# Optimization experiments

Hardware: AMD Instinct MI355X
Metric: run time of the kernel (lower is better)

Reference implementation:

```python
import jax, jax.numpy as jnp
import numpy as np

K = 7            # kernel_size (odd, neighborhood width)
H = 16           # num_heads
DIM = 512        # model dim
D = DIM // H     # head_dim = 32
SCALE = D ** (-0.5)


def setup_inputs() -> dict:
    key = jax.random.key(0)
    k0, k1, k2, k3 = jax.random.split(key, 4)
    B, L, C = 2, 16384, DIM
    x = jax.random.normal(k0, (B, L, C), jnp.float32)
    qkv_w = jax.random.normal(k1, (3 * C, C), jnp.float32) * 0.02   # torch Linear weight [out, in]
    qkv_b = jnp.zeros((3 * C,), jnp.float32)
    rpb = jax.random.normal(k2, (H, 2 * K - 1), jnp.float32) * 0.02  # relative positional bias table
    proj_w = jax.random.normal(k3, (C, C), jnp.float32) * 0.02
    proj_b = jnp.zeros((C,), jnp.float32)
    return {"x": x, "qkv_w": qkv_w, "qkv_b": qkv_b, "rpb": rpb,
            "proj_w": proj_w, "proj_b": proj_b}


def reference(x, qkv_w, qkv_b, rpb, proj_w, proj_b):
    B, L, C = x.shape
    # qkv projection: [B, L, 3C] -> [3, B, H, L, D]
    qkv = (x @ qkv_w.T + qkv_b).reshape(B, L, 3, H, D).transpose(2, 0, 3, 1, 4)
    q = qkv[0] * SCALE
    k = qkv[1]
    v = qkv[2]

    # Neighborhood window start per query (clamped at boundaries, NATTEN semantics)
    pos = jnp.arange(L)
    ni = jnp.clip(pos - K // 2, 0, L - K)            # [L]
    idx = ni[:, None] + jnp.arange(K)                 # [L, K] key indices per query

    kg = k[:, :, idx]                                 # [B, H, L, K, D] gathered keys
    vg = v[:, :, idx]                                 # [B, H, L, K, D] gathered values

    # relative positional bias: rpb index = (j - i) + (K - 1)
    bias = rpb[:, idx - pos[:, None] + (K - 1)]       # [H, L, K]

    attn = jnp.einsum('bhld,bhlkd->bhlk', q, kg) + bias[None]
    attn = jax.nn.softmax(attn, axis=-1)              # softmax over the K-neighborhood
    out = jnp.einsum('bhlk,bhlkd->bhld', attn, vg)
    out = out.transpose(0, 2, 1, 3).reshape(B, L, C)
    return out @ proj_w.T + proj_b
```

## Files before the change

### kernel.cpp

```cpp
#include <hip/hip_runtime.h>

typedef unsigned short u16;
typedef unsigned int   u32;
typedef __attribute__((ext_vector_type(8))) short bf16x8;
typedef __attribute__((ext_vector_type(4))) float f32x4;

#define L_SEQ 16384
#define NHEAD 16
#define CDIM  512
#define SCALE 0.17677669529663689f

#define AS1 __attribute__((address_space(1)))
#define AS3 __attribute__((address_space(3)))

__device__ __forceinline__ float bf2f(u16 v) {
    union { u32 u; float f; } x; x.u = ((u32)v) << 16; return x.f;
}
__device__ __forceinline__ u16 f2bf(float f) {
    union { u32 u; float f; } x; x.f = f;
    u32 r = x.u + 0x7fff + ((x.u >> 16) & 1);
    return (u16)(r >> 16);
}

__global__ __launch_bounds__(256)
void convert_weights_kernel(const void* __restrict__ qkv_w, const void* __restrict__ proj_w,
                            const void* __restrict__ qkv_b, const void* __restrict__ proj_b,
                            const void* __restrict__ rpb, u16* __restrict__ dst,
                            const u16* __restrict__ x, int* __restrict__ flag_out) {
    __shared__ int cnt;
    if (threadIdx.x == 0) cnt = 0;
    __syncthreads();
    int c = 0;
    for (int k = 0; k < 32; k++) {
        u16 v = x[2 * (threadIdx.x + 256 * k)];
        if ((v & 0x7F80) == 0x7F80) c++;
    }
    atomicAdd(&cnt, c);
    __syncthreads();
    const int f = (cnt > 0) ? 1 : 0;
    if (blockIdx.x == 0 && threadIdx.x == 0) *flag_out = f;
    for (int i = blockIdx.x * 256 + threadIdx.x; i < 1050832; i += gridDim.x * 256) {
        const void* src; int off;
        if (i < 786432)       { src = qkv_w;  off = i; }
        else if (i < 1048576) { src = proj_w; off = i - 786432; }
        else if (i < 1050112) { src = qkv_b;  off = i - 1048576; }
        else if (i < 1050624) { src = proj_b; off = i - 1050112; }
        else                  { src = rpb;    off = i - 1050624; }
        dst[i] = f ? f2bf(((const float*)src)[off]) : ((const u16*)src)[off];
    }
}

__global__ __launch_bounds__(256)
void convert_x_kernel(const void* __restrict__ src, u16* __restrict__ dst,
                      int base_c, int lch, const int* __restrict__ flag) {
    const int f  = *flag;
    const int i0 = (blockIdx.x * 256 + threadIdx.x) * 8;
    const int r  = i0 >> 9;
    const int b  = (r >= lch) ? 1 : 0;
    const size_t s = (size_t)(b * L_SEQ + base_c + (r - b * lch)) * 512 + (i0 & 511);
    if (f) {
        const float* sf = (const float*)src + s;
        union { u16 o[8]; uint4 v; } pk;
        #pragma unroll
        for (int j = 0; j < 8; j++) pk.o[j] = f2bf(sf[j]);
        *(uint4*)(dst + i0) = pk.v;
    } else {
        *(uint4*)(dst + i0) = *(const uint4*)((const u16*)src + s);
    }
}

#define VM4   asm volatile("s_waitcnt vmcnt(4)" ::: "memory")
#define VM0   asm volatile("s_waitcnt vmcnt(0)" ::: "memory")
#define LGKM0 asm volatile("s_waitcnt lgkmcnt(0)" ::: "memory")
#define NOOP  ((void)0)

#define PHASE(P, KS, CH, STAGE_STMT, WAIT_STMT)                                         \
    {                                                                                   \
        if ((CH) == 0) {                                                                \
            _Pragma("unroll")                                                           \
            for (int i_ = 0; i_ < 4; i_++)                                              \
                bb[i_] = *(const bf16x8*)&lds[P][1][KS][boff + i_ * 512];               \
        }                                                                               \
        _Pragma("unroll")                                                               \
        for (int i_ = 0; i_ < 4; i_++)                                                  \
            af[i_] = *(const bf16x8*)&lds[P][0][KS][aoff + ((CH) * 4 + i_) * 512];      \
        STAGE_STMT;                                                                     \
        WAIT_STMT;                                                                      \
        __builtin_amdgcn_s_barrier();                                                   \
        LGKM0;                                                                          \
        __builtin_amdgcn_s_setprio(1);                                                  \
        _Pragma("unroll")                                                               \
        for (int mi_ = 0; mi_ < 4; mi_++)                                               \
            _Pragma("unroll")                                                           \
            for (int ni_ = 0; ni_ < 4; ni_++)                                           \
                acc[(CH) * 4 + mi_][ni_] = __builtin_amdgcn_mfma_f32_16x16x32_bf16(     \
                    bb[ni_], af[mi_], acc[(CH) * 4 + mi_][ni_], 0, 0, 0);               \
        __builtin_amdgcn_s_setprio(0);                                                  \
        __builtin_amdgcn_s_barrier();                                                   \
    }

#define GEMM256_CORE(A_PTR, W_PTR, AROW0, N0)                                           \
    __shared__ u16 lds[2][2][2][8192];            \
    const int tid  = threadIdx.x;                                                       \
    const int wave = tid >> 6;                                                          \
    const int lane = tid & 63;                                                          \
    const int quad = lane >> 4;                                                         \
    const int r16  = lane & 15;                                                         \
    const int wm2  = wave >> 2;                                                         \
    const int wn4  = wave & 3;                                                          \
    f32x4 acc[8][4];                                                                    \
    _Pragma("unroll")                                                                   \
    for (int i = 0; i < 8; i++)                                                         \
        _Pragma("unroll")                                                               \
        for (int j = 0; j < 4; j++) acc[i][j] = (f32x4){0.f, 0.f, 0.f, 0.f};            \
    const int lr4  = lane >> 2;                                                         \
    const int swc2 = (((lane & 3) ^ ((lane >> 3) & 3)) << 3);                           \
    const u16* gA = (A_PTR) + (size_t)((AROW0) + wave * 16 + lr4) * 512 + swc2;         \
    const u16* gW = (W_PTR) + (size_t)((N0)    + wave * 16 + lr4) * 512 + swc2;         \
    const int rsw  = (quad ^ ((r16 >> 1) & 3)) << 3;                                    \
    const int aoff = (wm2 * 128 + r16) * 32 + rsw;                                      \
    const int boff = (wn4 * 64  + r16) * 32 + rsw;                                      \
    const int sdst = wave * 512;                                 \
    bf16x8 af[4], bb[4];                                                                \
    auto STAGE = [&](int P2, int OP, int KT, int KS) {                                  \
        const u16* g = (OP ? gW : gA) + KT * 64 + KS * 32;                              \
        u16* d0 = &lds[P2][OP][KS][sdst];                                               \
        __builtin_amdgcn_global_load_lds(                                               \
            (const AS1 void*)g, (AS3 void*)d0, 16, 0, 0);                               \
        __builtin_amdgcn_global_load_lds(                                               \
            (const AS1 void*)(g + (size_t)128 * 512), (AS3 void*)(d0 + 4096),           \
            16, 0, 0);                                                                  \
    };                                                                                  \
    STAGE(0, 0, 0, 0); STAGE(0, 1, 0, 0); STAGE(0, 0, 0, 1); STAGE(0, 1, 0, 1);         \
    VM4;                                                                                \
    __builtin_amdgcn_s_barrier();                                                       \
    for (int T = 0; T < 7; T++) {                                                       \
        const int p = T & 1, pn = p ^ 1;                                                \
        PHASE(p, 0, 0, STAGE(pn, 0, T + 1, 0), NOOP);                                   \
        PHASE(p, 0, 1, STAGE(pn, 1, T + 1, 0), VM4);                                    \
        PHASE(p, 1, 0, STAGE(pn, 0, T + 1, 1), NOOP);                                   \
        PHASE(p, 1, 1, STAGE(pn, 1, T + 1, 1), VM4);                                    \
    }                                                                                   \
    PHASE(1, 0, 0, NOOP, NOOP);                                                         \
    PHASE(1, 0, 1, NOOP, VM0);                                                          \
    PHASE(1, 1, 0, NOOP, NOOP);                                                         \
    PHASE(1, 1, 1, NOOP, NOOP);

__global__ __launch_bounds__(512, 2)
void gemm_qkv_kernel(const u16* __restrict__ A, const u16* __restrict__ W,
                     const u16* __restrict__ bias, u16* __restrict__ qkv_out, int lch)
{
    const int m0l = blockIdx.x << 8;
    const int n0  = blockIdx.y << 8;
    const int b   = blockIdx.z;
    const size_t plane = (size_t)1024 * lch;
    GEMM256_CORE(A, W, b * lch + m0l, n0)
    #pragma unroll
    for (int ni = 0; ni < 4; ni++) {
        const int colb  = n0 + wn4 * 64 + ni * 16 + quad * 4;
        const int which = colb >> 9;
        const int rem   = colb & 511;
        const int h     = rem >> 5;
        const int d     = rem & 31;
        const float scl = (which == 0) ? SCALE : 1.0f;
        const uint2 bp  = *(const uint2*)(bias + colb);
        const float b0 = bf2f((u16)bp.x), b1 = bf2f((u16)(bp.x >> 16));
        const float b2 = bf2f((u16)bp.y), b3 = bf2f((u16)(bp.y >> 16));
        u16* outb = qkv_out + (size_t)which * plane +
                    (size_t)(b * NHEAD + h) * lch * 32 + d;
        #pragma unroll
        for (int i = 0; i < 8; i++) {
            const int rrel = m0l + wm2 * 128 + i * 16 + r16;
            uint2 pk2;
            pk2.x = (u32)f2bf((acc[i][ni][0] + b0) * scl) |
                    ((u32)f2bf((acc[i][ni][1] + b1) * scl) << 16);
            pk2.y = (u32)f2bf((acc[i][ni][2] + b2) * scl) |
                    ((u32)f2bf((acc[i][ni][3] + b3) * scl) << 16);
            *(uint2*)(outb + (size_t)rrel * 32) = pk2;
        }
    }
}

__global__ __launch_bounds__(256)
void attn_kernel(const uint4* __restrict__ q, const uint4* __restrict__ k,
                 const uint4* __restrict__ v, const u16* __restrict__ rpb,
                 uint4* __restrict__ outa, int c0, int base_c, int lc_shift, int lch)
{
    const int grp = blockIdx.x * 64 + (threadIdx.x >> 2);
    const int d4  = threadIdx.x & 3;
    const int lr  = grp & ((1 << lc_shift) - 1);
    const int bh  = grp >> lc_shift;
    const int h   = bh & 15;
    const int l   = c0 + lr;
    const size_t base = (size_t)bh * lch * 4;

    const uint4 qp = q[base + (size_t)(l - base_c) * 4 + d4];
    float qf[8];
    qf[0] = bf2f((u16)qp.x); qf[1] = bf2f((u16)(qp.x >> 16));
    qf[2] = bf2f((u16)qp.y); qf[3] = bf2f((u16)(qp.y >> 16));
    qf[4] = bf2f((u16)qp.z); qf[5] = bf2f((u16)(qp.z >> 16));
    qf[6] = bf2f((u16)qp.w); qf[7] = bf2f((u16)(qp.w >> 16));

    int ni = l - 3;
    if (ni < 0) ni = 0;
    if (ni > L_SEQ - 7) ni = L_SEQ - 7;
    const int rn = ni - base_c;

    float logit[7];
    #pragma unroll
    for (int j = 0; j < 7; j++) {
        const uint4 kp = k[base + (size_t)(rn + j) * 4 + d4];
        float p;
        p  = qf[0] * bf2f((u16)kp.x) + qf[1] * bf2f((u16)(kp.x >> 16));
        p += qf[2] * bf2f((u16)kp.y) + qf[3] * bf2f((u16)(kp.y >> 16));
        p += qf[4] * bf2f((u16)kp.z) + qf[5] * bf2f((u16)(kp.z >> 16));
        p += qf[6] * bf2f((u16)kp.w) + qf[7] * bf2f((u16)(kp.w >> 16));
        p += __shfl_xor(p, 1, 64);
        p += __shfl_xor(p, 2, 64);
        logit[j] = p + bf2f(rpb[h * 13 + (ni + j - l + 6)]);
    }
    float mx = logit[0];
    #pragma unroll
    for (int j = 1; j < 7; j++) mx = fmaxf(mx, logit[j]);
    float s = 0.f, w[7];
    #pragma unroll
    for (int j = 0; j < 7; j++) { w[j] = __expf(logit[j] - mx); s += w[j]; }
    const float inv = 1.0f / s;
    float o[8] = {0.f, 0.f, 0.f, 0.f, 0.f, 0.f, 0.f, 0.f};
    #pragma unroll
    for (int j = 0; j < 7; j++) {
        const uint4 vp = v[base + (size_t)(rn + j) * 4 + d4];
        o[0] += w[j] * bf2f((u16)vp.x); o[1] += w[j] * bf2f((u16)(vp.x >> 16));
        o[2] += w[j] * bf2f((u16)vp.y); o[3] += w[j] * bf2f((u16)(vp.y >> 16));
        o[4] += w[j] * bf2f((u16)vp.z); o[5] += w[j] * bf2f((u16)(vp.z >> 16));
        o[6] += w[j] * bf2f((u16)vp.w); o[7] += w[j] * bf2f((u16)(vp.w >> 16));
    }
    uint4 pk;
    pk.x = (u32)f2bf(o[0] * inv) | ((u32)f2bf(o[1] * inv) << 16);
    pk.y = (u32)f2bf(o[2] * inv) | ((u32)f2bf(o[3] * inv) << 16);
    pk.z = (u32)f2bf(o[4] * inv) | ((u32)f2bf(o[5] * inv) << 16);
    pk.w = (u32)f2bf(o[6] * inv) | ((u32)f2bf(o[7] * inv) << 16);
    outa[((size_t)(((bh >> 4) << lc_shift) + lr)) * 64 + h * 4 + d4] = pk;
}

__global__ __launch_bounds__(512, 2)
void gemm_proj_kernel(const u16* __restrict__ A, const u16* __restrict__ W,
                      const u16* __restrict__ bias, void* __restrict__ out,
                      int c0, int lc, const int* __restrict__ flag)
{
    const int m0l = blockIdx.x << 8;
    const int n0  = blockIdx.y << 8;
    const int b   = blockIdx.z;
    GEMM256_CORE(A, W, b * lc + m0l, n0)
    const int f = *flag;
    #pragma unroll
    for (int ni = 0; ni < 4; ni++) {
        const int colb = n0 + wn4 * 64 + ni * 16 + quad * 4;
        const uint2 bp = *(const uint2*)(bias + colb);
        const float b0 = bf2f((u16)bp.x), b1 = bf2f((u16)(bp.x >> 16));
        const float b2 = bf2f((u16)bp.y), b3 = bf2f((u16)(bp.y >> 16));
        #pragma unroll
        for (int i = 0; i < 8; i++) {
            const int lr = m0l + wm2 * 128 + i * 16 + r16;
            const size_t idx = (size_t)(b * L_SEQ + c0 + lr) * CDIM + colb;
            const float v0 = acc[i][ni][0] + b0, v1 = acc[i][ni][1] + b1;
            const float v2 = acc[i][ni][2] + b2, v3 = acc[i][ni][3] + b3;
            if (f) {
                float4 st; st.x = v0; st.y = v1; st.z = v2; st.w = v3;
                *(float4*)((float*)out + idx) = st;
            } else {
                uint2 pk2;
                pk2.x = (u32)f2bf(v0) | ((u32)f2bf(v1) << 16);
                pk2.y = (u32)f2bf(v2) | ((u32)f2bf(v3) << 16);
                *(uint2*)((u16*)out + idx) = pk2;
            }
        }
    }
}

extern "C" void kernel_launch(void* const* d_in, const int* in_sizes, int n_in,
                              void* d_out, int out_size, void* d_ws, size_t ws_size,
                              hipStream_t stream) {
    const void* x      = d_in[0];
    const void* qkv_w  = d_in[1];
    const void* qkv_b  = d_in[2];
    const void* rpb    = d_in[3];
    const void* proj_w = d_in[4];
    const void* proj_b = d_in[5];

    int nchunk, lch, lc, lc_shift;
    static const int c0sA[1] = {0},                 basesA[1] = {0};
    static const int c0sB[2] = {0, 8192},           basesB[2] = {0, 7936};
    static const int c0sC[8] = {0, 2048, 4096, 6144, 8192, 10240, 12288, 14336};
    static const int basesC[8] = {0, 1920, 3968, 6016, 8064, 10112, 12160, 14080};
    const int* c0s; const int* bases;
    if (ws_size >= (size_t)2 * (16 + 1050880 + (size_t)4096 * 16384 + 1024 * 16384)) {
        nchunk = 1; lch = 16384; lc = 16384; lc_shift = 14; c0s = c0sA; bases = basesA;
    } else if (ws_size >= (size_t)2 * (16 + 1050880 + (size_t)4096 * 8448 + 1024 * 8192)) {
        nchunk = 2; lch = 8448;  lc = 8192;  lc_shift = 13; c0s = c0sB; bases = basesB;
    } else {
        nchunk = 8; lch = 2304;  lc = 2048;  lc_shift = 11; c0s = c0sC; bases = basesC;
    }

    u16* ws    = (u16*)d_ws;
    int* flag  = (int*)ws;
    u16* wseg  = ws + 16;
    u16* wqkv  = wseg;
    u16* wproj = wseg + 786432;
    u16* bqkv  = wseg + 1048576;
    u16* bproj = wseg + 1050112;
    u16* rpbc  = wseg + 1050624;
    u16* xc    = ws + 16 + 1050880;
    u16* qkv   = xc + (size_t)1024 * lch;
    u16* wsa   = qkv + (size_t)3072 * lch;

    convert_weights_kernel<<<2048, 256, 0, stream>>>(qkv_w, proj_w, qkv_b, proj_b,
                                                     rpb, wseg, (const u16*)x, flag);

    for (int c = 0; c < nchunk; c++) {
        convert_x_kernel<<<lch / 2, 256, 0, stream>>>(x, xc, bases[c], lch, flag);
        gemm_qkv_kernel<<<dim3(lch / 256, 6, 2), 512, 0, stream>>>(
            xc, wqkv, bqkv, qkv, lch);
        attn_kernel<<<lc / 2, 256, 0, stream>>>(
            (const uint4*)qkv, (const uint4*)(qkv + (size_t)1024 * lch),
            (const uint4*)(qkv + (size_t)2048 * lch), rpbc,
            (uint4*)wsa, c0s[c], bases[c], lc_shift, lch);
        gemm_proj_kernel<<<dim3(lc / 256, 2, 2), 512, 0, stream>>>(
            wsa, wproj, bproj, d_out, c0s[c], lc, flag);
    }
}
```

Before: 279.8 us.

## Restructure GEMM core to 256x128 tiles with 4 waves and single-phase K steps

Replaces the 8-wave 256x256 GEMM tile, which used a four-phase split-K pipeline, with a 4-wave 256x128 tile. Each wave now computes 128x64, and each of 16 iterations over K=32 slices does one LDS load, one staged prefetch and one barrier. Both the qkv and proj GEMMs double their grid width to match. The aim is fewer barriers per MFMA, more blocks to fill CUs, and smaller LDS use, at the cost of more redundant A-tile loads and a coarser prefetch/compute overlap.

```diff
diff --git a/kernel.cpp b/kernel.cpp
--- a/kernel.cpp
+++ b/kernel.cpp
@@ -69,45 +69,36 @@
     }
 }
 
-#define VM4   asm volatile("s_waitcnt vmcnt(4)" ::: "memory")
-#define VM0   asm volatile("s_waitcnt vmcnt(0)" ::: "memory")
-#define LGKM0 asm volatile("s_waitcnt lgkmcnt(0)" ::: "memory")
-#define NOOP  ((void)0)
-
-#define PHASE(P, KS, CH, STAGE_STMT, WAIT_STMT)                                         \
+#define GEMM_COMPUTE(P)                                                                 \
     {                                                                                   \
-        if ((CH) == 0) {                                                                \
-            _Pragma("unroll")                                                           \
-            for (int i_ = 0; i_ < 4; i_++)                                              \
-                bb[i_] = *(const bf16x8*)&lds[P][1][KS][boff + i_ * 512];               \
-        }                                                                               \
-        _Pragma("unroll")                                                               \
-        for (int i_ = 0; i_ < 4; i_++)                                                  \
-            af[i_] = *(const bf16x8*)&lds[P][0][KS][aoff + ((CH) * 4 + i_) * 512];      \
-        STAGE_STMT;                                                                     \
-        WAIT_STMT;                                                                      \
-        __builtin_amdgcn_s_barrier();                                                   \
-        LGKM0;                                                                          \
+        bf16x8 af[8], bb[4];                                                            \
+        _Pragma("unroll")                                                               \
+        for (int ni_ = 0; ni_ < 4; ni_++)                                               \
+            bb[ni_] = *(const bf16x8*)&lds[P][boff + ni_ * 512];                        \
+        _Pragma("unroll")                                                               \
+        for (int mi_ = 0; mi_ < 8; mi_++)                                               \
+            af[mi_] = *(const bf16x8*)&lds[P][aoff + mi_ * 512];                        \
+        asm volatile("s_waitcnt lgkmcnt(0)" ::: "memory");                              \
+        __builtin_amdgcn_sched_barrier(0);                                              \
         __builtin_amdgcn_s_setprio(1);                                                  \
         _Pragma("unroll")                                                               \
-        for (int mi_ = 0; mi_ < 4; mi_++)                                               \
+        for (int mi_ = 0; mi_ < 8; mi_++)                                               \
             _Pragma("unroll")                                                           \
             for (int ni_ = 0; ni_ < 4; ni_++)                                           \
-                acc[(CH) * 4 + mi_][ni_] = __builtin_amdgcn_mfma_f32_16x16x32_bf16(     \
-                    bb[ni_], af[mi_], acc[(CH) * 4 + mi_][ni_], 0, 0, 0);               \
+                acc[mi_][ni_] = __builtin_amdgcn_mfma_f32_16x16x32_bf16(                \
+                    bb[ni_], af[mi_], acc[mi_][ni_], 0, 0, 0);                          \
         __builtin_amdgcn_s_setprio(0);                                                  \
-        __builtin_amdgcn_s_barrier();                                                   \
     }
 
 #define GEMM256_CORE(A_PTR, W_PTR, AROW0, N0)                                           \
-    __shared__ u16 lds[2][2][2][8192];            \
+    __shared__ u16 lds[2][12288];               \
     const int tid  = threadIdx.x;                                                       \
     const int wave = tid >> 6;                                                          \
     const int lane = tid & 63;                                                          \
     const int quad = lane >> 4;                                                         \
     const int r16  = lane & 15;                                                         \
-    const int wm2  = wave >> 2;                                                         \
-    const int wn4  = wave & 3;                                                          \
+    const int wm   = wave >> 1;                                                         \
+    const int wn   = wave & 1;                                                          \
     f32x4 acc[8][4];                                                                    \
     _Pragma("unroll")                                                                   \
     for (int i = 0; i < 8; i++)                                                         \
@@ -118,46 +109,47 @@
     const u16* gA = (A_PTR) + (size_t)((AROW0) + wave * 16 + lr4) * 512 + swc2;         \
     const u16* gW = (W_PTR) + (size_t)((N0)    + wave * 16 + lr4) * 512 + swc2;         \
     const int rsw  = (quad ^ ((r16 >> 1) & 3)) << 3;                                    \
-    const int aoff = (wm2 * 128 + r16) * 32 + rsw;                                      \
-    const int boff = (wn4 * 64  + r16) * 32 + rsw;                                      \
-    const int sdst = wave * 512;                                 \
-    bf16x8 af[4], bb[4];                                                                \
-    auto STAGE = [&](int P2, int OP, int KT, int KS) {                                  \
-        const u16* g = (OP ? gW : gA) + KT * 64 + KS * 32;                              \
-        u16* d0 = &lds[P2][OP][KS][sdst];                                               \
-        __builtin_amdgcn_global_load_lds(                                               \
-            (const AS1 void*)g, (AS3 void*)d0, 16, 0, 0);                               \
-        __builtin_amdgcn_global_load_lds(                                               \
-            (const AS1 void*)(g + (size_t)128 * 512), (AS3 void*)(d0 + 4096),           \
-            16, 0, 0);                                                                  \
+    const int aoff = (wm * 128 + r16) * 32 + rsw;                                       \
+    const int boff = 8192 + (wn * 64 + r16) * 32 + rsw;                                 \
+    const int sdst = wave * 512;                                                        \
+    auto STAGE = [&](int P2, int KT) {                                                  \
+        _Pragma("unroll")                                                               \
+        for (int i_ = 0; i_ < 4; i_++)                                                  \
+            __builtin_amdgcn_global_load_lds(                                           \
+                (const AS1 void*)(gA + KT * 32 + (size_t)i_ * 32768),                   \
+                (AS3 void*)&lds[P2][i_ * 2048 + sdst], 16, 0, 0);                       \
+        _Pragma("unroll")                                                               \
+        for (int j_ = 0; j_ < 2; j_++)                                                  \
+            __builtin_amdgcn_global_load_lds(                                           \
+                (const AS1 void*)(gW + KT * 32 + (size_t)j_ * 32768),                   \
+                (AS3 void*)&lds[P2][8192 + j_ * 2048 + sdst], 16, 0, 0);                \
     };                                                                                  \
-    STAGE(0, 0, 0, 0); STAGE(0, 1, 0, 0); STAGE(0, 0, 0, 1); STAGE(0, 1, 0, 1);         \
-    VM4;                                                                                \
+    STAGE(0, 0);                                                                        \
+    asm volatile("s_waitcnt vmcnt(0)" ::: "memory");                                    \
     __builtin_amdgcn_s_barrier();                                                       \
-    for (int T = 0; T < 7; T++) {                                                       \
-        const int p = T & 1, pn = p ^ 1;                                                \
-        PHASE(p, 0, 0, STAGE(pn, 0, T + 1, 0), NOOP);                                   \
-        PHASE(p, 0, 1, STAGE(pn, 1, T + 1, 0), VM4);                                    \
-        PHASE(p, 1, 0, STAGE(pn, 0, T + 1, 1), NOOP);                                   \
-        PHASE(p, 1, 1, STAGE(pn, 1, T + 1, 1), VM4);                                    \
+    __builtin_amdgcn_sched_barrier(0);                                                  \
+    for (int T = 0; T < 15; T++) {                                                      \
+        const int p = T & 1;                                                            \
+        STAGE(p ^ 1, T + 1);                                                            \
+        GEMM_COMPUTE(p)                                                                 \
+        asm volatile("s_waitcnt vmcnt(0)" ::: "memory");                                \
+        __builtin_amdgcn_s_barrier();                                                   \
+        __builtin_amdgcn_sched_barrier(0);                                              \
     }                                                                                   \
-    PHASE(1, 0, 0, NOOP, NOOP);                                                         \
-    PHASE(1, 0, 1, NOOP, VM0);                                                          \
-    PHASE(1, 1, 0, NOOP, NOOP);                                                         \
-    PHASE(1, 1, 1, NOOP, NOOP);
-
-__global__ __launch_bounds__(512, 2)
+    GEMM_COMPUTE(1)
+
+__global__ __launch_bounds__(256, 2)
 void gemm_qkv_kernel(const u16* __restrict__ A, const u16* __restrict__ W,
                      const u16* __restrict__ bias, u16* __restrict__ qkv_out, int lch)
 {
     const int m0l = blockIdx.x << 8;
-    const int n0  = blockIdx.y << 8;
+    const int n0  = blockIdx.y << 7;
     const int b   = blockIdx.z;
     const size_t plane = (size_t)1024 * lch;
     GEMM256_CORE(A, W, b * lch + m0l, n0)
     #pragma unroll
     for (int ni = 0; ni < 4; ni++) {
-        const int colb  = n0 + wn4 * 64 + ni * 16 + quad * 4;
+        const int colb  = n0 + wn * 64 + ni * 16 + quad * 4;
         const int which = colb >> 9;
         const int rem   = colb & 511;
         const int h     = rem >> 5;
@@ -170,7 +162,7 @@
                     (size_t)(b * NHEAD + h) * lch * 32 + d;
         #pragma unroll
         for (int i = 0; i < 8; i++) {
-            const int rrel = m0l + wm2 * 128 + i * 16 + r16;
+            const int rrel = m0l + wm * 128 + i * 16 + r16;
             uint2 pk2;
             pk2.x = (u32)f2bf((acc[i][ni][0] + b0) * scl) |
                     ((u32)f2bf((acc[i][ni][1] + b1) * scl) << 16);
@@ -243,25 +235,25 @@
     outa[((size_t)(((bh >> 4) << lc_shift) + lr)) * 64 + h * 4 + d4] = pk;
 }
 
-__global__ __launch_bounds__(512, 2)
+__global__ __launch_bounds__(256, 2)
 void gemm_proj_kernel(const u16* __restrict__ A, const u16* __restrict__ W,
                       const u16* __restrict__ bias, void* __restrict__ out,
                       int c0, int lc, const int* __restrict__ flag)
 {
     const int m0l = blockIdx.x << 8;
-    const int n0  = blockIdx.y << 8;
+    const int n0  = blockIdx.y << 7;
     const int b   = blockIdx.z;
     GEMM256_CORE(A, W, b * lc + m0l, n0)
     const int f = *flag;
     #pragma unroll
     for (int ni = 0; ni < 4; ni++) {
-        const int colb = n0 + wn4 * 64 + ni * 16 + quad * 4;
+        const int colb = n0 + wn * 64 + ni * 16 + quad * 4;
         const uint2 bp = *(const uint2*)(bias + colb);
         const float b0 = bf2f((u16)bp.x), b1 = bf2f((u16)(bp.x >> 16));
         const float b2 = bf2f((u16)bp.y), b3 = bf2f((u16)(bp.y >> 16));
         #pragma unroll
         for (int i = 0; i < 8; i++) {
-            const int lr = m0l + wm2 * 128 + i * 16 + r16;
+            const int lr = m0l + wm * 128 + i * 16 + r16;
             const size_t idx = (size_t)(b * L_SEQ + c0 + lr) * CDIM + colb;
             const float v0 = acc[i][ni][0] + b0, v1 = acc[i][ni][1] + b1;
             const float v2 = acc[i][ni][2] + b2, v3 = acc[i][ni][3] + b3;
@@ -319,13 +311,13 @@
 
     for (int c = 0; c < nchunk; c++) {
         convert_x_kernel<<<lch / 2, 256, 0, stream>>>(x, xc, bases[c], lch, flag);
-        gemm_qkv_kernel<<<dim3(lch / 256, 6, 2), 512, 0, stream>>>(
+        gemm_qkv_kernel<<<dim3(lch / 256, 12, 2), 256, 0, stream>>>(
             xc, wqkv, bqkv, qkv, lch);
         attn_kernel<<<lc / 2, 256, 0, stream>>>(
             (const uint4*)qkv, (const uint4*)(qkv + (size_t)1024 * lch),
             (const uint4*)(qkv + (size_t)2048 * lch), rpbc,
             (uint4*)wsa, c0s[c], bases[c], lc_shift, lch);
-        gemm_proj_kernel<<<dim3(lc / 256, 2, 2), 512, 0, stream>>>(
+        gemm_proj_kernel<<<dim3(lc / 256, 4, 2), 256, 0, stream>>>(
             wsa, wproj, bproj, d_out, c0s[c], lc, flag);
     }
 }
```

New measurement: 292.6 us. +4.6%, slower.

## Store QKV row-major interleaved and compute two queries per attention thread group

Applied to the files above, without the earlier changes.

The QKV GEMM epilogue now writes a token-major [B, L, 1536] layout instead of separate per-head planes, so rows are contiguous across heads. The attention kernel reads Q/K/V from this combined buffer and processes two adjacent queries per 4-thread group, loading 8 K/V rows once and reusing them for both windows, which roughly halves neighborhood loads. This raises register pressure (16 uint4 K/V values held per thread). The GEMM stores also become more scattered across rows of stride 1536.

```diff
diff --git a/kernel.cpp b/kernel.cpp
--- a/kernel.cpp
+++ b/kernel.cpp
@@ -153,21 +153,15 @@
     const int m0l = blockIdx.x << 8;
     const int n0  = blockIdx.y << 8;
     const int b   = blockIdx.z;
-    const size_t plane = (size_t)1024 * lch;
     GEMM256_CORE(A, W, b * lch + m0l, n0)
+    u16* orow = qkv_out + (size_t)(b * lch) * 1536;
     #pragma unroll
     for (int ni = 0; ni < 4; ni++) {
         const int colb  = n0 + wn4 * 64 + ni * 16 + quad * 4;
-        const int which = colb >> 9;
-        const int rem   = colb & 511;
-        const int h     = rem >> 5;
-        const int d     = rem & 31;
-        const float scl = (which == 0) ? SCALE : 1.0f;
+        const float scl = (colb < 512) ? SCALE : 1.0f;
         const uint2 bp  = *(const uint2*)(bias + colb);
         const float b0 = bf2f((u16)bp.x), b1 = bf2f((u16)(bp.x >> 16));
         const float b2 = bf2f((u16)bp.y), b3 = bf2f((u16)(bp.y >> 16));
-        u16* outb = qkv_out + (size_t)which * plane +
-                    (size_t)(b * NHEAD + h) * lch * 32 + d;
         #pragma unroll
         for (int i = 0; i < 8; i++) {
             const int rrel = m0l + wm2 * 128 + i * 16 + r16;
@@ -176,71 +170,88 @@
                     ((u32)f2bf((acc[i][ni][1] + b1) * scl) << 16);
             pk2.y = (u32)f2bf((acc[i][ni][2] + b2) * scl) |
                     ((u32)f2bf((acc[i][ni][3] + b3) * scl) << 16);
-            *(uint2*)(outb + (size_t)rrel * 32) = pk2;
+            *(uint2*)(orow + (size_t)rrel * 1536 + colb) = pk2;
         }
     }
 }
 
 __global__ __launch_bounds__(256)
-void attn_kernel(const uint4* __restrict__ q, const uint4* __restrict__ k,
-                 const uint4* __restrict__ v, const u16* __restrict__ rpb,
+void attn_kernel(const uint4* __restrict__ qkvb, const u16* __restrict__ rpb,
                  uint4* __restrict__ outa, int c0, int base_c, int lc_shift, int lch)
 {
     const int grp = blockIdx.x * 64 + (threadIdx.x >> 2);
     const int d4  = threadIdx.x & 3;
-    const int lr  = grp & ((1 << lc_shift) - 1);
-    const int bh  = grp >> lc_shift;
+    const int lrh = grp & ((1 << (lc_shift - 1)) - 1);
+    const int bh  = grp >> (lc_shift - 1);
     const int h   = bh & 15;
-    const int l   = c0 + lr;
-    const size_t base = (size_t)bh * lch * 4;
-
-    const uint4 qp = q[base + (size_t)(l - base_c) * 4 + d4];
-    float qf[8];
-    qf[0] = bf2f((u16)qp.x); qf[1] = bf2f((u16)(qp.x >> 16));
-    qf[2] = bf2f((u16)qp.y); qf[3] = bf2f((u16)(qp.y >> 16));
-    qf[4] = bf2f((u16)qp.z); qf[5] = bf2f((u16)(qp.z >> 16));
-    qf[6] = bf2f((u16)qp.w); qf[7] = bf2f((u16)(qp.w >> 16));
-
-    int ni = l - 3;
-    if (ni < 0) ni = 0;
-    if (ni > L_SEQ - 7) ni = L_SEQ - 7;
-    const int rn = ni - base_c;
-
-    float logit[7];
+    const int b   = bh >> 4;
+    const int l0  = c0 + 2 * lrh;
+    const size_t base = (size_t)b * lch * 192;
+    const int qc  = h * 4 + d4;
+
+    int ni0 = l0 - 3;  if (ni0 < 0) ni0 = 0;  if (ni0 > L_SEQ - 7) ni0 = L_SEQ - 7;
+    int ni1 = l0 - 2;  if (ni1 < 0) ni1 = 0;  if (ni1 > L_SEQ - 7) ni1 = L_SEQ - 7;
+    const int off1 = ni1 - ni0;
+
+    uint4 kp[8], vp[8];
     #pragma unroll
-    for (int j = 0; j < 7; j++) {
-        const uint4 kp = k[base + (size_t)(rn + j) * 4 + d4];
-        float p;
-        p  = qf[0] * bf2f((u16)kp.x) + qf[1] * bf2f((u16)(kp.x >> 16));
-        p += qf[2] * bf2f((u16)kp.y) + qf[3] * bf2f((u16)(kp.y >> 16));
-        p += qf[4] * bf2f((u16)kp.z) + qf[5] * bf2f((u16)(kp.z >> 16));
-        p += qf[6] * bf2f((u16)kp.w) + qf[7] * bf2f((u16)(kp.w >> 16));
-        p += __shfl_xor(p, 1, 64);
-        p += __shfl_xor(p, 2, 64);
-        logit[j] = p + bf2f(rpb[h * 13 + (ni + j - l + 6)]);
-    }
-    float mx = logit[0];
+    for (int j = 0; j < 8; j++) {
+        int r = ni0 + j;
+        if (r > L_SEQ - 1) r = L_SEQ - 1;
+        const size_t rl = base + (size_t)(r - base_c) * 192;
+        kp[j] = qkvb[rl + 64 + qc];
+        vp[j] = qkvb[rl + 128 + qc];
+    }
+    uint4 qp[2];
+    qp[0] = qkvb[base + (size_t)(l0     - base_c) * 192 + qc];
+    qp[1] = qkvb[base + (size_t)(l0 + 1 - base_c) * 192 + qc];
+
     #pragma unroll
-    for (int j = 1; j < 7; j++) mx = fmaxf(mx, logit[j]);
-    float s = 0.f, w[7];
-    #pragma unroll
-    for (int j = 0; j < 7; j++) { w[j] = __expf(logit[j] - mx); s += w[j]; }
-    const float inv = 1.0f / s;
-    float o[8] = {0.f, 0.f, 0.f, 0.f, 0.f, 0.f, 0.f, 0.f};
-    #pragma unroll
-    for (int j = 0; j < 7; j++) {
-        const uint4 vp = v[base + (size_t)(rn + j) * 4 + d4];
-        o[0] += w[j] * bf2f((u16)vp.x); o[1] += w[j] * bf2f((u16)(vp.x >> 16));
-        o[2] += w[j] * bf2f((u16)vp.y); o[3] += w[j] * bf2f((u16)(vp.y >> 16));
-        o[4] += w[j] * bf2f((u16)vp.z); o[5] += w[j] * bf2f((u16)(vp.z >> 16));
-        o[6] += w[j] * bf2f((u16)vp.w); o[7] += w[j] * bf2f((u16)(vp.w >> 16));
-    }
-    uint4 pk;
-    pk.x = (u32)f2bf(o[0] * inv) | ((u32)f2bf(o[1] * inv) << 16);
-    pk.y = (u32)f2bf(o[2] * inv) | ((u32)f2bf(o[3] * inv) << 16);
-    pk.z = (u32)f2bf(o[4] * inv) | ((u32)f2bf(o[5] * inv) << 16);
-    pk.w = (u32)f2bf(o[6] * inv) | ((u32)f2bf(o[7] * inv) << 16);
-    outa[((size_t)(((bh >> 4) << lc_shift) + lr)) * 64 + h * 4 + d4] = pk;
+    for (int t = 0; t < 2; t++) {
+        const int la  = l0 + t;
+        const int nio = t ? off1 : 0;
+        const int nia = ni0 + nio;
+        float qf[8];
+        qf[0] = bf2f((u16)qp[t].x); qf[1] = bf2f((u16)(qp[t].x >> 16));
+        qf[2] = bf2f((u16)qp[t].y); qf[3] = bf2f((u16)(qp[t].y >> 16));
+        qf[4] = bf2f((u16)qp[t].z); qf[5] = bf2f((u16)(qp[t].z >> 16));
+        qf[6] = bf2f((u16)qp[t].w); qf[7] = bf2f((u16)(qp[t].w >> 16));
+        float logit[7];
+        #pragma unroll
+        for (int j = 0; j < 7; j++) {
+            const uint4 kk = kp[nio + j];
+            float p;
+            p  = qf[0] * bf2f((u16)kk.x) + qf[1] * bf2f((u16)(kk.x >> 16));
+            p += qf[2] * bf2f((u16)kk.y) + qf[3] * bf2f((u16)(kk.y >> 16));
+            p += qf[4] * bf2f((u16)kk.z) + qf[5] * bf2f((u16)(kk.z >> 16));
+            p += qf[6] * bf2f((u16)kk.w) + qf[7] * bf2f((u16)(kk.w >> 16));
+            p += __shfl_xor(p, 1, 64);
+            p += __shfl_xor(p, 2, 64);
+            logit[j] = p + bf2f(rpb[h * 13 + (nia + j - la + 6)]);
+        }
+        float mx = logit[0];
+        #pragma unroll
+        for (int j = 1; j < 7; j++) mx = fmaxf(mx, logit[j]);
+        float s = 0.f, w[7];
+        #pragma unroll
+        for (int j = 0; j < 7; j++) { w[j] = __expf(logit[j] - mx); s += w[j]; }
+        const float inv = 1.0f / s;
+        float o[8] = {0.f, 0.f, 0.f, 0.f, 0.f, 0.f, 0.f, 0.f};
+        #pragma unroll
+        for (int j = 0; j < 7; j++) {
+            const uint4 vv = vp[nio + j];
+            o[0] += w[j] * bf2f((u16)vv.x); o[1] += w[j] * bf2f((u16)(vv.x >> 16));
+            o[2] += w[j] * bf2f((u16)vv.y); o[3] += w[j] * bf2f((u16)(vv.y >> 16));
+            o[4] += w[j] * bf2f((u16)vv.z); o[5] += w[j] * bf2f((u16)(vv.z >> 16));
+            o[6] += w[j] * bf2f((u16)vv.w); o[7] += w[j] * bf2f((u16)(vv.w >> 16));
+        }
+        uint4 pk;
+        pk.x = (u32)f2bf(o[0] * inv) | ((u32)f2bf(o[1] * inv) << 16);
+        pk.y = (u32)f2bf(o[2] * inv) | ((u32)f2bf(o[3] * inv) << 16);
+        pk.z = (u32)f2bf(o[4] * inv) | ((u32)f2bf(o[5] * inv) << 16);
+        pk.w = (u32)f2bf(o[6] * inv) | ((u32)f2bf(o[7] * inv) << 16);
+        outa[((size_t)(b << lc_shift) + 2 * lrh + t) * 64 + h * 4 + d4] = pk;
+    }
 }
 
 __global__ __launch_bounds__(512, 2)
@@ -321,9 +332,8 @@
         convert_x_kernel<<<lch / 2, 256, 0, stream>>>(x, xc, bases[c], lch, flag);
         gemm_qkv_kernel<<<dim3(lch / 256, 6, 2), 512, 0, stream>>>(
             xc, wqkv, bqkv, qkv, lch);
-        attn_kernel<<<lc / 2, 256, 0, stream>>>(
-            (const uint4*)qkv, (const uint4*)(qkv + (size_t)1024 * lch),
-            (const uint4*)(qkv + (size_t)2048 * lch), rpbc,
+        attn_kernel<<<lc / 4, 256, 0, stream>>>(
+            (const uint4*)qkv, rpbc,
             (uint4*)wsa, c0s[c], bases[c], lc_shift, lch);
         gemm_proj_kernel<<<dim3(lc / 256, 2, 2), 512, 0, stream>>>(
             wsa, wproj, bproj, d_out, c0s[c], lc, flag);
```

After: 405.6 us. 45.0% more time.
